# Performance work log

Hardware: AMD Instinct MI355X
Metric: run time of the kernel (lower is better)

Reference implementation:

```python
import jax, jax.numpy as jnp
import numpy as np

B, T, A, H, E = 512, 64, 32, 512, 32


def sinusoidal_pos_encoding(t, dim):
    # t: (B, T) float positions -> (B, T, dim)
    half = dim // 2
    freqs = jnp.exp(-jnp.log(10000.0) * jnp.arange(half, dtype=jnp.float32) / half)
    ang = t[..., None] * freqs  # (B, T, half)
    return jnp.concatenate([jnp.sin(ang), jnp.cos(ang)], axis=-1)


def cat_linear(x, W, b, cat_ids):
    # x: (B, T, Din); W: (E, Din, Dout); b: (E, Dout); cat_ids: (B,)
    Wg = W[cat_ids]            # (B, Din, Dout) gathered per-sample weights
    bg = b[cat_ids][:, None]   # (B, 1, Dout)
    return jnp.einsum('btd,bdh->bth', x, Wg) + bg


def swish(x):
    return x * jax.nn.sigmoid(x)


def setup_inputs() -> dict:
    key = jax.random.key(0)
    ks = jax.random.split(key, 10)
    s = lambda fan_in: 1.0 / np.sqrt(fan_in)
    return {
        'actions': jax.random.normal(ks[0], (B, T, A), dtype=jnp.float32),
        'timesteps': jax.random.uniform(ks[1], (B,), dtype=jnp.float32),
        'cat_ids': jax.random.randint(ks[2], (B,), 0, E),
        'W1': jax.random.normal(ks[3], (E, A, H), dtype=jnp.float32) * s(A),
        'b1': jnp.zeros((E, H), dtype=jnp.float32),
        'W2': jax.random.normal(ks[4], (E, 2 * H, H), dtype=jnp.float32) * s(2 * H),
        'b2': jnp.zeros((E, H), dtype=jnp.float32),
        'W3': jax.random.normal(ks[5], (E, H, H), dtype=jnp.float32) * s(H),
        'b3': jnp.zeros((E, H), dtype=jnp.float32),
    }


def reference(actions, timesteps, cat_ids, W1, b1, W2, b2, W3, b3):
    b, t, _ = actions.shape
    timesteps_bt = jnp.broadcast_to(timesteps[:, None], (b, t))
    a_emb = cat_linear(actions, W1, b1, cat_ids)              # (B, T, H)
    tau_emb = sinusoidal_pos_encoding(timesteps_bt, H).astype(a_emb.dtype)
    x = jnp.concatenate([a_emb, tau_emb], axis=-1)            # (B, T, 2H)
    x = swish(cat_linear(x, W2, b2, cat_ids))                 # (B, T, H)
    x = cat_linear(x, W3, b3, cat_ids)                        # (B, T, H)
    return x
```

## Files before the change

### kernel.cpp

```cpp
#include <hip/hip_runtime.h>
#include <hip/hip_bf16.h>

#define B_ 512
#define T_ 64
#define A_ 32
#define H_ 512
#define E_ 32
#define MAX_TASKS 272
#define CAP_ 168
#define GRID_ (8 * CAP_)

typedef unsigned short u16;
typedef unsigned int u32;
typedef __attribute__((ext_vector_type(8))) short short8;
typedef __attribute__((ext_vector_type(4))) float floatx4;

static __device__ __forceinline__ u16 f2bf(float f) {
    u32 u = __builtin_bit_cast(u32, f);
    u += 0x7fffu + ((u >> 16) & 1u);
    return (u16)(u >> 16);
}

static __device__ __forceinline__ void gl2lds16(const u16* g, u16* l) {
    __builtin_amdgcn_global_load_lds(
        (const __attribute__((address_space(1))) void*)g,
        (__attribute__((address_space(3))) void*)l, 16, 0, 0);
}

__global__ __launch_bounds__(512) void embed_group_kernel(
        const float* __restrict__ actions, const float* __restrict__ timesteps,
        const int* __restrict__ cat_ids, const float* __restrict__ W1,
        const float* __restrict__ b1,
        u16* __restrict__ a_emb, float* __restrict__ tauG,
        int* __restrict__ sample_list, int4* __restrict__ tasks,
        int* __restrict__ itemlist, int* __restrict__ eoff_g,
        int* __restrict__ ecnt_g) {
    int tid = threadIdx.x;

    if (blockIdx.x == B_) {
        __shared__ int cnt[E_], off[E_], cur[E_], toff[E_], jc[8];
        __shared__ int total, fb;
        if (tid < E_) { cnt[tid] = 0; cur[tid] = 0; }
        __syncthreads();
        int e = cat_ids[tid];
        atomicAdd(&cnt[e], 1);
        __syncthreads();
        if (tid == 0) {
            int run = 0, trun = 0;
            for (int i = 0; i < E_; i++) {
                off[i] = run;  run += cnt[i];
                toff[i] = trun; trun += (cnt[i] + 1) >> 1;
            }
            total = trun;
        }
        __syncthreads();
        if (tid < E_) {
            int c = cnt[tid], o = off[tid], to = toff[tid];
            eoff_g[tid] = o;
            ecnt_g[tid] = c;
            for (int j = 0; j < c; j += 2)
                tasks[to++] = make_int4(tid, o + j, (c - j >= 2) ? 2 : 1, 0);
        }
        if (tid < 8) {
            int J = 0;
            for (int cc = 0; cc < 4; cc++)
                J += 4 * ((cnt[tid + 8 * cc] + 1) >> 1);
            jc[tid] = J;
        }
        __syncthreads();
        if (tid == 0) {
            int f = 0;
            for (int x = 0; x < 8; x++) if (jc[x] > CAP_) f = 1;
            fb = f;
        }
        __syncthreads();
        if (!fb) {
            if (tid < 8) {
                int j = 0;
                for (int cc = 0; cc < 4; cc++) {
                    int ee = tid + 8 * cc;
                    int nt = (cnt[ee] + 1) >> 1, t0 = toff[ee];
                    for (int t = t0; t < t0 + nt; t++)
                        for (int nb = 0; nb < 4; nb++) {
                            itemlist[tid + 8 * j] = (t << 2) | nb;
                            j++;
                        }
                }
                for (; j < CAP_; j++) itemlist[tid + 8 * j] = -1;
            }
        } else {
            for (int f = tid; f < GRID_; f += 512)
                itemlist[f] = (f < 4 * total) ? f : -1;
        }
        int p = atomicAdd(&cur[e], 1);
        sample_list[off[e] + p] = tid;
        return;
    }

    int b = blockIdx.x;
    int e = cat_ids[b];
    {
        float tval = timesteps[b];
        int kk = tid & 255;
        float freq = expf(-9.210340371976184f * (float)kk * (1.0f / 256.0f));
        float ang = tval * freq;
        tauG[(size_t)b * H_ + tid] = (tid < 256) ? sinf(ang) : cosf(ang);
    }

    __shared__ float act[T_ * A_];
    const float* asrc = actions + (size_t)b * T_ * A_;
    for (int i = tid; i < T_ * A_; i += 512) act[i] = asrc[i];
    __syncthreads();

    const float* w1 = W1 + (size_t)e * A_ * H_;
    float wcol[A_];
#pragma unroll
    for (int k = 0; k < A_; k++) wcol[k] = w1[k * H_ + tid];
    float bb = b1[e * H_ + tid];
    u16* orow = a_emb + (size_t)b * T_ * H_;
    for (int tt = 0; tt < T_; tt++) {
        float acc = bb;
#pragma unroll
        for (int k = 0; k < A_; k++)
            acc = fmaf(act[tt * A_ + k], wcol[k], acc);
        orow[tt * H_ + tid] = f2bf(acc);
    }
}

static __device__ __forceinline__ void ct_block32(
        const float* __restrict__ W, u16* __restrict__ Wt,
        int srcK, int dstK, int e, int k0, int n) {
    const float* src = W + ((size_t)e * srcK + k0) * H_ + n;
    short8 out[4];
#pragma unroll
    for (int j = 0; j < 32; j++)
        out[j >> 3][j & 7] = (short)f2bf(src[(size_t)j * H_]);
    u16* dst = Wt + ((size_t)e * H_ + n) * dstK + k0;
#pragma unroll
    for (int c = 0; c < 4; c++) *(short8*)(dst + c * 8) = out[c];
}

__global__ __launch_bounds__(256) void convert_transpose(
        const float* __restrict__ W, u16* __restrict__ Wt, int srcK, int dstK) {
    ct_block32(W, Wt, srcK, dstK, blockIdx.z, blockIdx.x * 32,
               blockIdx.y * 256 + threadIdx.x);
}

__global__ __launch_bounds__(256) void prep_kernel(
        const float* __restrict__ W2, u16* __restrict__ Wt2a,
        const float* __restrict__ tauG, const float* __restrict__ b2,
        const int* __restrict__ sample_list,
        const int* __restrict__ eoff, const int* __restrict__ ecnt,
        float* __restrict__ bias2s) {
    int tid = threadIdx.x;
    int bid = blockIdx.x;

    __shared__ float tauT[512][20];

    if (bid < 1024) {
        int e = bid >> 5, sub = bid & 31;
        ct_block32(W2, Wt2a, 2 * H_, H_, e, (sub & 15) * 32,
                   (sub >> 4) * 256 + tid);
        return;
    }

    int id = bid - 1024;
    int cc = id & 7;
    int e  = id >> 3;
    int cnt = ecnt[e], off = eoff[e];
    if (cnt == 0) return;
    int wv = tid >> 6, ln = tid & 63;
    int n = cc * 64 + ln;
    const float* wb = W2 + ((size_t)e * 1024 + 512) * H_ + n;
    float bcol = b2[e * H_ + n];

    for (int c0 = 0; c0 < cnt; c0 += 16) {
        for (int i = tid; i < 16 * 512; i += 256) {
            int sl = i >> 9, k = i & 511;
            float v = 0.f;
            if (c0 + sl < cnt)
                v = tauG[(size_t)sample_list[off + c0 + sl] * H_ + k];
            tauT[k][sl] = v;
        }
        __syncthreads();

        float a0 = 0.f, a1 = 0.f, a2 = 0.f, a3 = 0.f;
#pragma unroll 8
        for (int k = 0; k < 512; k++) {
            float w = wb[(size_t)k * H_];
            float4 t4 = *(const float4*)&tauT[k][wv * 4];
            a0 = fmaf(t4.x, w, a0);
            a1 = fmaf(t4.y, w, a1);
            a2 = fmaf(t4.z, w, a2);
            a3 = fmaf(t4.w, w, a3);
        }

#pragma unroll
        for (int si = 0; si < 4; si++) {
            int sl = wv * 4 + si;
            if (c0 + sl < cnt) {
                int s = sample_list[off + c0 + sl];
                float av = (si == 0) ? a0 : (si == 1) ? a1 : (si == 2) ? a2 : a3;
                bias2s[(size_t)s * H_ + n] = av + bcol;
            }
        }
        __syncthreads();
    }
}

template <int DIN, bool PSBIAS, bool DO_SWISH, bool OUT_BF16>
__global__ __launch_bounds__(256, 2) void moe_gemm(
        const u16* __restrict__ xsrc, const u16* __restrict__ Wt,
        const float* __restrict__ bias,
        const int* __restrict__ sample_list, const int4* __restrict__ tasks,
        const int* __restrict__ itemlist, void* __restrict__ outp) {
    int item = itemlist[blockIdx.x];
    if (item < 0) return;
    int4 task = tasks[item >> 2];
    int nb = item & 3;
    int ns = task.z;
    int e = task.x;
    int s0 = sample_list[task.y];
    int s1 = (ns > 1) ? sample_list[task.y + 1] : s0;
    int n0 = nb * 128;

    int tid = threadIdx.x;
    int lane = tid & 63, wv = tid >> 6;
    int wr = wv >> 1, wc = wv & 1;
    int quad = lane >> 4, c15 = lane & 15;
    int r8 = lane >> 3, cg = lane & 7;

    __shared__ __align__(16) u16 xs[2][128 * 64];
    __shared__ __align__(16) u16 wt[2][128 * 64];

    floatx4 acc[4][4];
    floatx4 zero4 = {0.f, 0.f, 0.f, 0.f};
#pragma unroll
    for (int i = 0; i < 4; i++)
#pragma unroll
        for (int j = 0; j < 4; j++) acc[i][j] = zero4;

    const u16* wbase = Wt + (size_t)(e * H_ + n0) * DIN;
    int kc_sw = (cg ^ r8) * 8;

    auto stage = [&](int b, int k0) {
#pragma unroll
        for (int h = 0; h < 4; h++) {
            int rbase = h * 32 + wv * 8;
            int s = (h < 2) ? s0 : s1;
            int t = (rbase + r8) & 63;
            gl2lds16(xsrc + ((size_t)s * T_ + t) * H_ + k0 + kc_sw,
                     &xs[b][rbase * 64]);
        }
#pragma unroll
        for (int h = 0; h < 4; h++) {
            int nbase = h * 32 + wv * 8;
            gl2lds16(wbase + (size_t)(nbase + r8) * DIN + k0 + kc_sw,
                     &wt[b][nbase * 64]);
        }
    };

    auto compute = [&](int b) {
#pragma unroll
        for (int kk = 0; kk < 2; kk++) {
            int c = kk * 4 + quad;
            short8 af[4], bfr[4];
#pragma unroll
            for (int i = 0; i < 4; i++) {
                int row = wr * 64 + i * 16 + c15;
                af[i] = *(const short8*)&xs[b][row * 64 + ((c ^ (row & 7)) * 8)];
                int nr = wc * 64 + i * 16 + c15;
                bfr[i] = *(const short8*)&wt[b][nr * 64 + ((c ^ (nr & 7)) * 8)];
            }
#pragma unroll
            for (int mt = 0; mt < 4; mt++)
#pragma unroll
                for (int nt = 0; nt < 4; nt++)
                    acc[mt][nt] = __builtin_amdgcn_mfma_f32_16x16x32_bf16(
                            af[mt], bfr[nt], acc[mt][nt], 0, 0, 0);
        }
    };

    constexpr int KI = DIN / 64;
    stage(0, 0);
    stage(1, 64);
    asm volatile("s_waitcnt vmcnt(8)" ::: "memory");
    __builtin_amdgcn_s_barrier();
    __builtin_amdgcn_sched_barrier(0);
#pragma unroll
    for (int t = 0; t < KI; ++t) {
        compute(t & 1);
        if (t + 1 < KI) {
            __builtin_amdgcn_s_barrier();
            __builtin_amdgcn_sched_barrier(0);
            if (t + 2 < KI) {
                stage(t & 1, (t + 2) * 64);
                asm volatile("s_waitcnt vmcnt(8)" ::: "memory");
            } else {
                asm volatile("s_waitcnt vmcnt(0)" ::: "memory");
            }
            __builtin_amdgcn_s_barrier();
            __builtin_amdgcn_sched_barrier(0);
        }
    }

    if (wr >= ns) return;
    int s = (wr == 0) ? s0 : s1;
    const float* bp = PSBIAS ? (bias + (size_t)s * H_)
                             : (bias + (size_t)e * H_);
#pragma unroll
    for (int mt = 0; mt < 4; mt++) {
        int tb = mt * 16 + quad * 4;
#pragma unroll
        for (int nt = 0; nt < 4; nt++) {
            int col = n0 + wc * 64 + nt * 16 + c15;
            float bv = bp[col];
#pragma unroll
            for (int r = 0; r < 4; r++) {
                float v = acc[mt][nt][r] + bv;
                if (DO_SWISH) v = v / (1.0f + expf(-v));
                size_t oidx = ((size_t)s * T_ + tb + r) * H_ + col;
                if (OUT_BF16) ((u16*)outp)[oidx] = f2bf(v);
                else          ((float*)outp)[oidx] = v;
            }
        }
    }
}

extern "C" void kernel_launch(void* const* d_in, const int* in_sizes, int n_in,
                              void* d_out, int out_size, void* d_ws, size_t ws_size,
                              hipStream_t stream) {
    const float* actions   = (const float*)d_in[0];
    const float* timesteps = (const float*)d_in[1];
    const int*   cat_ids   = (const int*)d_in[2];
    const float* W1 = (const float*)d_in[3];
    const float* b1 = (const float*)d_in[4];
    const float* W2 = (const float*)d_in[5];
    const float* b2 = (const float*)d_in[6];
    const float* W3 = (const float*)d_in[7];
    const float* b3 = (const float*)d_in[8];

    char* ws = (char*)d_ws;
    u16* a_emb = (u16*)ws;
    u16* y     = (u16*)(ws + (size_t)32 * 1024 * 1024);
    char* meta = ws + (size_t)64 * 1024 * 1024 + 512 * 1024;
    int*  sample_list = (int*)meta;
    int4* tasks       = (int4*)(meta + 8192);
    int*  itemlist    = (int*)(meta + 16384);
    int*  eoff        = (int*)(meta + 24576);
    int*  ecnt        = (int*)(meta + 24576 + 128);
    u16*  Wt2a   = (u16*)d_out;
    float* bias2s = (float*)((char*)d_out + (size_t)48 * 1024 * 1024);
    float* tauG   = (float*)((char*)d_out + (size_t)52 * 1024 * 1024);
    u16*  Wt3    = a_emb;

    hipLaunchKernelGGL(embed_group_kernel, dim3(B_ + 1), dim3(512), 0, stream,
                       actions, timesteps, cat_ids, W1, b1,
                       a_emb, tauG,
                       sample_list, tasks, itemlist, eoff, ecnt);
    hipLaunchKernelGGL(prep_kernel, dim3(1280), dim3(256), 0, stream,
                       W2, Wt2a, tauG, b2, sample_list, eoff, ecnt, bias2s);
    hipLaunchKernelGGL((moe_gemm<H_, true, true, true>), dim3(GRID_),
                       dim3(256), 0, stream,
                       a_emb, Wt2a, bias2s, sample_list, tasks, itemlist,
                       (void*)y);
    hipLaunchKernelGGL(convert_transpose, dim3(H_ / 32, 2, E_), dim3(256),
                       0, stream, W3, Wt3, H_, H_);
    hipLaunchKernelGGL((moe_gemm<H_, false, false, false>), dim3(GRID_),
                       dim3(256), 0, stream,
                       y, Wt3, b3, sample_list, tasks, itemlist, d_out);
}
```

Measured before the change: 349.4 us.

## Fold W3 conversion into prep kernel and restructure tau bias GEMV per sample

The separate W3 convert-transpose launch is merged into prep_kernel, which now has 2560 blocks covering the W2 and W3 bf16 transposes, and buffers are relocated so Wt3 no longer aliases a_emb. The tau-bias computation changes from per-expert column blocks that loop over sample chunks to per-sample groups of four with float4 weight loads, a K split across half-waves, and a shuffle reduction. Blocks are indexed with an XCD-aware mapping. This removes one launch and balances the bias work across experts, at the cost of rereading W2 weights once per sample instead of once per expert.

```diff
diff --git a/kernel.cpp b/kernel.cpp
--- a/kernel.cpp
+++ b/kernel.cpp
@@ -140,71 +140,78 @@
     for (int c = 0; c < 4; c++) *(short8*)(dst + c * 8) = out[c];
 }
 
-__global__ __launch_bounds__(256) void convert_transpose(
-        const float* __restrict__ W, u16* __restrict__ Wt, int srcK, int dstK) {
-    ct_block32(W, Wt, srcK, dstK, blockIdx.z, blockIdx.x * 32,
-               blockIdx.y * 256 + threadIdx.x);
-}
-
 __global__ __launch_bounds__(256) void prep_kernel(
-        const float* __restrict__ W2, u16* __restrict__ Wt2a,
+        const float* __restrict__ W2, const float* __restrict__ W3,
+        u16* __restrict__ Wt2a, u16* __restrict__ Wt3,
         const float* __restrict__ tauG, const float* __restrict__ b2,
-        const int* __restrict__ sample_list,
-        const int* __restrict__ eoff, const int* __restrict__ ecnt,
+        const int* __restrict__ cat_ids, const int* __restrict__ sample_list,
         float* __restrict__ bias2s) {
     int tid = threadIdx.x;
     int bid = blockIdx.x;
 
-    __shared__ float tauT[512][20];
-
-    if (bid < 1024) {
-        int e = bid >> 5, sub = bid & 31;
-        ct_block32(W2, Wt2a, 2 * H_, H_, e, (sub & 15) * 32,
-                   (sub >> 4) * 256 + tid);
+    __shared__ float tauLds[4][512];
+
+    if (bid >= 512) {
+        int local = bid - 512;
+        if (local < 1024) {
+            int e = local >> 5, sub = local & 31;
+            ct_block32(W2, Wt2a, 2 * H_, H_, e, (sub & 15) * 32,
+                       (sub >> 4) * 256 + tid);
+        } else {
+            local -= 1024;
+            int e = local >> 5, sub = local & 31;
+            ct_block32(W3, Wt3, H_, H_, e, (sub & 15) * 32,
+                       (sub >> 4) * 256 + tid);
+        }
         return;
     }
 
-    int id = bid - 1024;
-    int cc = id & 7;
-    int e  = id >> 3;
-    int cnt = ecnt[e], off = eoff[e];
-    if (cnt == 0) return;
-    int wv = tid >> 6, ln = tid & 63;
-    int n = cc * 64 + ln;
-    const float* wb = W2 + ((size_t)e * 1024 + 512) * H_ + n;
-    float bcol = b2[e * H_ + n];
-
-    for (int c0 = 0; c0 < cnt; c0 += 16) {
-        for (int i = tid; i < 16 * 512; i += 256) {
-            int sl = i >> 9, k = i & 511;
-            float v = 0.f;
-            if (c0 + sl < cnt)
-                v = tauG[(size_t)sample_list[off + c0 + sl] * H_ + k];
-            tauT[k][sl] = v;
-        }
-        __syncthreads();
-
-        float a0 = 0.f, a1 = 0.f, a2 = 0.f, a3 = 0.f;
-#pragma unroll 8
-        for (int k = 0; k < 512; k++) {
-            float w = wb[(size_t)k * H_];
-            float4 t4 = *(const float4*)&tauT[k][wv * 4];
-            a0 = fmaf(t4.x, w, a0);
-            a1 = fmaf(t4.y, w, a1);
-            a2 = fmaf(t4.z, w, a2);
-            a3 = fmaf(t4.w, w, a3);
-        }
-
-#pragma unroll
-        for (int si = 0; si < 4; si++) {
-            int sl = wv * 4 + si;
-            if (c0 + sl < cnt) {
-                int s = sample_list[off + c0 + sl];
-                float av = (si == 0) ? a0 : (si == 1) ? a1 : (si == 2) ? a2 : a3;
-                bias2s[(size_t)s * H_ + n] = av + bcol;
-            }
-        }
-        __syncthreads();
+    int xcd = bid & 7, jj = bid >> 3;
+    int u = xcd * 64 + jj;
+    int g = u >> 2, q = u & 3;
+
+    for (int i = tid; i < 4 * 512; i += 256) {
+        int sl = i >> 9, k = i & 511;
+        tauLds[sl][k] = tauG[(size_t)sample_list[g * 4 + sl] * H_ + k];
+    }
+    __syncthreads();
+
+    int wv = tid >> 6, lane = tid & 63;
+    int l = lane & 31, kh = lane >> 5;
+    int s = sample_list[g * 4 + wv];
+    int e = cat_ids[s];
+    const float* wb = W2 + ((size_t)e * 1024 + 512 + kh * 256) * H_
+                      + q * 128 + l * 4;
+    const float* tp = &tauLds[wv][kh * 256];
+
+    float4 acc = {0.f, 0.f, 0.f, 0.f};
+#pragma unroll 2
+    for (int k4 = 0; k4 < 256; k4 += 4) {
+        float4 t4 = *(const float4*)&tp[k4];
+        float4 w0 = *(const float4*)(wb + (size_t)(k4 + 0) * H_);
+        float4 w1 = *(const float4*)(wb + (size_t)(k4 + 1) * H_);
+        float4 w2 = *(const float4*)(wb + (size_t)(k4 + 2) * H_);
+        float4 w3 = *(const float4*)(wb + (size_t)(k4 + 3) * H_);
+        acc.x = fmaf(t4.x, w0.x, acc.x); acc.y = fmaf(t4.x, w0.y, acc.y);
+        acc.z = fmaf(t4.x, w0.z, acc.z); acc.w = fmaf(t4.x, w0.w, acc.w);
+        acc.x = fmaf(t4.y, w1.x, acc.x); acc.y = fmaf(t4.y, w1.y, acc.y);
+        acc.z = fmaf(t4.y, w1.z, acc.z); acc.w = fmaf(t4.y, w1.w, acc.w);
+        acc.x = fmaf(t4.z, w2.x, acc.x); acc.y = fmaf(t4.z, w2.y, acc.y);
+        acc.z = fmaf(t4.z, w2.z, acc.z); acc.w = fmaf(t4.z, w2.w, acc.w);
+        acc.x = fmaf(t4.w, w3.x, acc.x); acc.y = fmaf(t4.w, w3.y, acc.y);
+        acc.z = fmaf(t4.w, w3.z, acc.z); acc.w = fmaf(t4.w, w3.w, acc.w);
+    }
+
+    acc.x += __shfl_xor(acc.x, 32, 64);
+    acc.y += __shfl_xor(acc.y, 32, 64);
+    acc.z += __shfl_xor(acc.z, 32, 64);
+    acc.w += __shfl_xor(acc.w, 32, 64);
+
+    if (kh == 0) {
+        int n = q * 128 + l * 4;
+        float4 bv = *(const float4*)(b2 + (size_t)e * H_ + n);
+        float4 outv = {acc.x + bv.x, acc.y + bv.y, acc.z + bv.z, acc.w + bv.w};
+        *(float4*)&bias2s[(size_t)s * H_ + n] = outv;
     }
 }
 
@@ -341,7 +348,7 @@
     const float* b3 = (const float*)d_in[8];
 
     char* ws = (char*)d_ws;
-    u16* a_emb = (u16*)ws;
+    u16* Wt3   = (u16*)ws;
     u16* y     = (u16*)(ws + (size_t)32 * 1024 * 1024);
     char* meta = ws + (size_t)64 * 1024 * 1024 + 512 * 1024;
     int*  sample_list = (int*)meta;
@@ -350,22 +357,21 @@
     int*  eoff        = (int*)(meta + 24576);
     int*  ecnt        = (int*)(meta + 24576 + 128);
     u16*  Wt2a   = (u16*)d_out;
+    u16*  a_emb  = (u16*)((char*)d_out + (size_t)16 * 1024 * 1024);
     float* bias2s = (float*)((char*)d_out + (size_t)48 * 1024 * 1024);
-    float* tauG   = (float*)((char*)d_out + (size_t)52 * 1024 * 1024);
-    u16*  Wt3    = a_emb;
+    float* tauG   = (float*)((char*)d_out + (size_t)49 * 1024 * 1024);
 
     hipLaunchKernelGGL(embed_group_kernel, dim3(B_ + 1), dim3(512), 0, stream,
                        actions, timesteps, cat_ids, W1, b1,
                        a_emb, tauG,
                        sample_list, tasks, itemlist, eoff, ecnt);
-    hipLaunchKernelGGL(prep_kernel, dim3(1280), dim3(256), 0, stream,
-                       W2, Wt2a, tauG, b2, sample_list, eoff, ecnt, bias2s);
+    hipLaunchKernelGGL(prep_kernel, dim3(2560), dim3(256), 0, stream,
+                       W2, W3, Wt2a, Wt3, tauG, b2, cat_ids, sample_list,
+                       bias2s);
     hipLaunchKernelGGL((moe_gemm<H_, true, true, true>), dim3(GRID_),
                        dim3(256), 0, stream,
                        a_emb, Wt2a, bias2s, sample_list, tasks, itemlist,
                        (void*)y);
-    hipLaunchKernelGGL(convert_transpose, dim3(H_ / 32, 2, E_), dim3(256),
-                       0, stream, W3, Wt3, H_, H_);
     hipLaunchKernelGGL((moe_gemm<H_, false, false, false>), dim3(GRID_),
                        dim3(256), 0, stream,
                        y, Wt3, b3, sample_list, tasks, itemlist, d_out);
```

New measurement: 286.1 us. 18.1% less time.
